# Performance work log

Hardware: AMD Instinct MI355X
Metric: run time of the kernel (lower is better)

The kernel has to match this reference:

```python
import jax, jax.numpy as jnp
import numpy as np

N = 12288
IN_DIM = 128
OUT_DIM = 128
LR_SLOPE = 0.01
NEG_INF = -9e16


def setup_inputs() -> dict:
    key = jax.random.key(0)
    k1, k2, k3, k4 = jax.random.split(key, 4)
    emb_mat = jax.random.normal(k1, (N, IN_DIM), dtype=jnp.float32)
    adj_mat = jax.random.randint(k2, (N, N), 0, 2, dtype=jnp.int32)
    # xavier-normal-ish init for params
    W = jax.random.normal(k3, (OUT_DIM, IN_DIM), dtype=jnp.float32) * (2.0 / (IN_DIM + OUT_DIM)) ** 0.5
    a = jax.random.normal(k4, (2 * OUT_DIM, 1), dtype=jnp.float32) * (2.0 / (2 * OUT_DIM + 1)) ** 0.5
    return {"emb_mat": emb_mat, "adj_mat": adj_mat, "W": W, "a": a}


def reference(emb_mat, adj_mat, W, a):
    out_dim = W.shape[0]
    e_new = emb_mat @ W.T                       # [N, D_out]
    a1 = a[:out_dim, :]                         # [D_out, 1]
    a2 = a[out_dim:, :]                         # [D_out, 1]
    source_scores = e_new @ a1                  # [N, 1]
    target_scores = e_new @ a2                  # [N, 1]
    e = source_scores + target_scores.T         # [N, N] outer sum
    e = jax.nn.leaky_relu(e, negative_slope=LR_SLOPE)
    e = jnp.where(adj_mat > 0, e, NEG_INF)
    attention = jax.nn.softmax(e, axis=-1)      # [N, N]
    e_transf = attention @ e_new                # [N, D_out]
    return jax.nn.relu(e_transf)
```

## Files before the change

### kernel.cpp

```cpp
#include <hip/hip_runtime.h>


#define NN 12288
#define DIM 128
#define CSPLIT 8
#define COLS_PER (NN / CSPLIT)
#define BK 32
#define NCHUNK (COLS_PER / BK)

typedef __bf16 bf16x8 __attribute__((ext_vector_type(8)));
typedef float f32x4 __attribute__((ext_vector_type(4)));

__global__ __launch_bounds__(256) void k1_gemm(const float* __restrict__ emb,
                                               const float* __restrict__ W,
                                               const float* __restrict__ a,
                                               __bf16* __restrict__ Vt,
                                               float* __restrict__ s,
                                               float* __restrict__ t) {
  const int lane = threadIdx.x & 63;
  const int wave = threadIdx.x >> 6;
  const int m = lane & 15;
  const int quad = lane >> 4;
  const int row0 = blockIdx.x * 64 + wave * 16;

  f32x4 acc[8];
#pragma unroll
  for (int nb = 0; nb < 8; nb++) acc[nb] = (f32x4){0.f, 0.f, 0.f, 0.f};

#pragma unroll
  for (int ks = 0; ks < 4; ks++) {
    const int k0 = ks * 32 + quad * 8;
    const float* ep = emb + (size_t)(row0 + m) * DIM + k0;
    float4 lo = *(const float4*)ep;
    float4 hi = *(const float4*)(ep + 4);
    bf16x8 af = {(__bf16)lo.x, (__bf16)lo.y, (__bf16)lo.z, (__bf16)lo.w,
                 (__bf16)hi.x, (__bf16)hi.y, (__bf16)hi.z, (__bf16)hi.w};
#pragma unroll
    for (int nb = 0; nb < 8; nb++) {
      const float* wp = W + (size_t)(nb * 16 + m) * DIM + k0;
      float4 wlo = *(const float4*)wp;
      float4 whi = *(const float4*)(wp + 4);
      bf16x8 bf = {(__bf16)wlo.x, (__bf16)wlo.y, (__bf16)wlo.z, (__bf16)wlo.w,
                   (__bf16)whi.x, (__bf16)whi.y, (__bf16)whi.z, (__bf16)whi.w};
      acc[nb] = __builtin_amdgcn_mfma_f32_16x16x32_bf16(af, bf, acc[nb], 0, 0, 0);
    }
  }

  float a1v[8], a2v[8];
#pragma unroll
  for (int nb = 0; nb < 8; nb++) {
    a1v[nb] = a[nb * 16 + m];
    a2v[nb] = a[DIM + nb * 16 + m];
  }
#pragma unroll
  for (int r = 0; r < 4; r++) {
    const int gr = row0 + quad * 4 + r;
    float ps = 0.f, pt = 0.f;
#pragma unroll
    for (int nb = 0; nb < 8; nb++) {
      float e = acc[nb][r];
      ps += e * a1v[nb];
      pt += e * a2v[nb];
      Vt[(size_t)(nb * 16 + m) * NN + gr] = (__bf16)e;
    }
    ps += __shfl_xor(ps, 1); ps += __shfl_xor(ps, 2);
    ps += __shfl_xor(ps, 4); ps += __shfl_xor(ps, 8);
    pt += __shfl_xor(pt, 1); pt += __shfl_xor(pt, 2);
    pt += __shfl_xor(pt, 4); pt += __shfl_xor(pt, 8);
    if (m == 0) { s[gr] = ps; t[gr] = pt; }
  }
}

__global__ __launch_bounds__(256) void ktmax(const float* __restrict__ t,
                                             float* __restrict__ tmax) {
  __shared__ float red[256];
  float mx = -1e30f;
  for (int i = threadIdx.x; i < NN; i += 256) mx = fmaxf(mx, t[i]);
  red[threadIdx.x] = mx;
  __syncthreads();
  for (int off = 128; off; off >>= 1) {
    if ((int)threadIdx.x < off) red[threadIdx.x] = fmaxf(red[threadIdx.x], red[threadIdx.x + off]);
    __syncthreads();
  }
  if (threadIdx.x == 0) *tmax = red[0];
}

__global__ __launch_bounds__(256, 3) void k2_attn(const int* __restrict__ adj,
                                                  const __bf16* __restrict__ Vt,
                                                  const float* __restrict__ s,
                                                  const float* __restrict__ t,
                                                  const float* __restrict__ tmaxp,
                                                  float* __restrict__ part,
                                                  float* __restrict__ lpart) {
  __shared__ unsigned long long adjb[2][128][5];
  __shared__ __attribute__((aligned(16))) __bf16 vtb[2][128][40];

  const int tid = threadIdx.x;
  const int lane = tid & 63;
  const int wave = tid >> 6;
  const int m = lane & 15;
  const int quad = lane >> 4;
  const int row0 = blockIdx.x * 128;
  const int cs = blockIdx.y;
  const int col0 = cs * COLS_PER;
  const int rowA = row0 + wave * 32 + m;
  const int rowB = rowA + 16;

  const float Tmax = *tmaxp;
  const float sA = s[rowA], sB = s[rowB];
  const float uA = sA + Tmax, uB = sB + Tmax;
  const float mA = fmaxf(uA, 0.01f * uA);
  const float mB = fmaxf(uB, 0.01f * uB);

  f32x4 accA[8], accB[8];
#pragma unroll
  for (int nb = 0; nb < 8; nb++) {
    accA[nb] = (f32x4){0.f, 0.f, 0.f, 0.f};
    accB[nb] = (f32x4){0.f, 0.f, 0.f, 0.f};
  }
  float lA = 0.f, lB = 0.f;

  int4 ga[4];
  bf16x8 gv[2];
  const int fr = tid >> 3, fc = (tid & 7) * 4;
  const int vd = tid >> 2, vc = (tid & 3) * 8;

  auto fetch = [&](int c) {
    const int cc = col0 + c * BK;
#pragma unroll
    for (int p = 0; p < 4; p++)
      ga[p] = *(const int4*)(adj + (size_t)(row0 + fr + p * 32) * NN + cc + fc);
#pragma unroll
    for (int p = 0; p < 2; p++)
      gv[p] = *(const bf16x8*)(Vt + (size_t)(vd + p * 64) * NN + cc + vc);
  };
  auto commit = [&](int b) {
#pragma unroll
    for (int p = 0; p < 4; p++) {
      unsigned pk = (unsigned)(ga[p].x != 0) | ((unsigned)(ga[p].y != 0) << 8) |
                    ((unsigned)(ga[p].z != 0) << 16) | ((unsigned)(ga[p].w != 0) << 24);
      *(unsigned*)((unsigned char*)&adjb[b][fr + p * 32][0] + fc) = pk;
    }
#pragma unroll
    for (int p = 0; p < 2; p++)
      *(bf16x8*)&vtb[b][vd + p * 64][vc] = gv[p];
  };

  fetch(0);
  commit(0);
  __syncthreads();

  for (int c = 0; c < NCHUNK; c++) {
    if (c + 1 < NCHUNK) fetch(c + 1);

    const int b = c & 1;
    const float* tp = t + col0 + c * BK + quad * 8;
    float4 ct0 = *(const float4*)tp;
    float4 ct1 = *(const float4*)(tp + 4);
    unsigned long long avA = adjb[b][wave * 32 + m][quad];
    unsigned long long avB = adjb[b][wave * 32 + 16 + m][quad];

    bf16x8 pA, pB;
#define PEL(frag, jj, tv, av, ss, mm, ll)                               \
    {                                                                   \
      float v = (ss) + (tv);                                            \
      float lv = fmaxf(v, 0.01f * v);                                   \
      float e = (((av) >> (8 * (jj))) & 1) ? __expf(lv - (mm)) : 0.f;   \
      (ll) += e;                                                        \
      frag[jj] = (__bf16)e;                                             \
    }
    PEL(pA, 0, ct0.x, avA, sA, mA, lA)
    PEL(pA, 1, ct0.y, avA, sA, mA, lA)
    PEL(pA, 2, ct0.z, avA, sA, mA, lA)
    PEL(pA, 3, ct0.w, avA, sA, mA, lA)
    PEL(pA, 4, ct1.x, avA, sA, mA, lA)
    PEL(pA, 5, ct1.y, avA, sA, mA, lA)
    PEL(pA, 6, ct1.z, avA, sA, mA, lA)
    PEL(pA, 7, ct1.w, avA, sA, mA, lA)
    PEL(pB, 0, ct0.x, avB, sB, mB, lB)
    PEL(pB, 1, ct0.y, avB, sB, mB, lB)
    PEL(pB, 2, ct0.z, avB, sB, mB, lB)
    PEL(pB, 3, ct0.w, avB, sB, mB, lB)
    PEL(pB, 4, ct1.x, avB, sB, mB, lB)
    PEL(pB, 5, ct1.y, avB, sB, mB, lB)
    PEL(pB, 6, ct1.z, avB, sB, mB, lB)
    PEL(pB, 7, ct1.w, avB, sB, mB, lB)
#undef PEL

#pragma unroll
    for (int nb = 0; nb < 8; nb++) {
      bf16x8 bv = *(const bf16x8*)&vtb[b][nb * 16 + m][quad * 8];
      accA[nb] = __builtin_amdgcn_mfma_f32_16x16x32_bf16(pA, bv, accA[nb], 0, 0, 0);
      accB[nb] = __builtin_amdgcn_mfma_f32_16x16x32_bf16(pB, bv, accB[nb], 0, 0, 0);
    }

    if (c + 1 < NCHUNK) commit((c + 1) & 1);
    __syncthreads();
  }

  lA += __shfl_xor(lA, 16); lA += __shfl_xor(lA, 32);
  lB += __shfl_xor(lB, 16); lB += __shfl_xor(lB, 32);
  if (quad == 0) {
    lpart[(size_t)cs * NN + rowA] = lA;
    lpart[(size_t)cs * NN + rowB] = lB;
  }

  float* po = part + ((size_t)cs * NN + row0 + wave * 32) * DIM;
#pragma unroll
  for (int nb = 0; nb < 8; nb++) {
#pragma unroll
    for (int r = 0; r < 4; r++) {
      po[(size_t)(quad * 4 + r) * DIM + nb * 16 + m] = accA[nb][r];
      po[(size_t)(16 + quad * 4 + r) * DIM + nb * 16 + m] = accB[nb][r];
    }
  }
}

__global__ __launch_bounds__(256) void kl(const float* __restrict__ lpart,
                                          float* __restrict__ linv) {
  const int r = blockIdx.x * 256 + threadIdx.x;
  float l = 0.f;
#pragma unroll
  for (int cs = 0; cs < CSPLIT; cs++) l += lpart[(size_t)cs * NN + r];
  linv[r] = 1.0f / l;
}

__global__ __launch_bounds__(256) void k3_fin(const float* __restrict__ part,
                                              const float* __restrict__ linv,
                                              float* __restrict__ out) {
  const int idx = blockIdx.x * 256 + threadIdx.x;
  const int row = idx >> 5;
  const float4* p4 = (const float4*)part;
  float4 acc = p4[idx];
#pragma unroll
  for (int cs = 1; cs < CSPLIT; cs++) {
    float4 v = p4[(size_t)cs * (NN * DIM / 4) + idx];
    acc.x += v.x; acc.y += v.y; acc.z += v.z; acc.w += v.w;
  }
  const float li = linv[row];
  float4 o;
  o.x = fmaxf(acc.x * li, 0.f);
  o.y = fmaxf(acc.y * li, 0.f);
  o.z = fmaxf(acc.z * li, 0.f);
  o.w = fmaxf(acc.w * li, 0.f);
  ((float4*)out)[idx] = o;
}

extern "C" void kernel_launch(void* const* d_in, const int* in_sizes, int n_in,
                              void* d_out, int out_size, void* d_ws, size_t ws_size,
                              hipStream_t stream) {
  (void)in_sizes; (void)n_in; (void)out_size; (void)ws_size;
  const float* emb = (const float*)d_in[0];
  const int* adj = (const int*)d_in[1];
  const float* W = (const float*)d_in[2];
  const float* a = (const float*)d_in[3];
  float* out = (float*)d_out;

  char* ws = (char*)d_ws;
  __bf16* Vt = (__bf16*)ws;
  float* s = (float*)(ws + 3145728);
  float* t = (float*)(ws + 3194880);
  float* lpart = (float*)(ws + 3244032);
  float* linv = (float*)(ws + 3637248);
  float* tmax = (float*)(ws + 3686400);
  float* part = (float*)(ws + 3686656);

  k1_gemm<<<NN / 64, 256, 0, stream>>>(emb, W, a, Vt, s, t);
  ktmax<<<1, 256, 0, stream>>>(t, tmax);
  dim3 g2(NN / 128, CSPLIT);
  k2_attn<<<g2, 256, 0, stream>>>(adj, Vt, s, t, tmax, part, lpart);
  kl<<<NN / 256, 256, 0, stream>>>(lpart, linv);
  k3_fin<<<NN * DIM / 4 / 256, 256, 0, stream>>>(part, linv, out);
}
```

Baseline: 823.3 us.

## Fuse tmax and l-reduction into neighbor kernels and deepen prefetch pipeline

Removes the single-block ktmax kernel by computing the column-score max with an atomicMax on a biased float-as-uint in k1, launched with one wave per block. The kl kernel is folded into k3_fin, which reduces the row sums in shared memory. k2_attn now prefetches two chunks ahead in registers, including the t values, and skips the final barrier. The aim is to cut launch and serial-kernel overhead and hide global latency, at the cost of more registers in k2 and a +64 bias that assumes t > -64 for the uint ordering.

```diff
diff --git a/kernel.cpp b/kernel.cpp
--- a/kernel.cpp
+++ b/kernel.cpp
@@ -11,17 +11,17 @@
 typedef __bf16 bf16x8 __attribute__((ext_vector_type(8)));
 typedef float f32x4 __attribute__((ext_vector_type(4)));
 
-__global__ __launch_bounds__(256) void k1_gemm(const float* __restrict__ emb,
-                                               const float* __restrict__ W,
-                                               const float* __restrict__ a,
-                                               __bf16* __restrict__ Vt,
-                                               float* __restrict__ s,
-                                               float* __restrict__ t) {
-  const int lane = threadIdx.x & 63;
-  const int wave = threadIdx.x >> 6;
+__global__ __launch_bounds__(64) void k1_gemm(const float* __restrict__ emb,
+                                              const float* __restrict__ W,
+                                              const float* __restrict__ a,
+                                              __bf16* __restrict__ Vt,
+                                              float* __restrict__ s,
+                                              float* __restrict__ t,
+                                              unsigned* __restrict__ tmax) {
+  const int lane = threadIdx.x;
   const int m = lane & 15;
   const int quad = lane >> 4;
-  const int row0 = blockIdx.x * 64 + wave * 16;
+  const int row0 = blockIdx.x * 16;
 
   f32x4 acc[8];
 #pragma unroll
@@ -52,6 +52,7 @@
     a1v[nb] = a[nb * 16 + m];
     a2v[nb] = a[DIM + nb * 16 + m];
   }
+  float tm_local = 0.f;
 #pragma unroll
   for (int r = 0; r < 4; r++) {
     const int gr = row0 + quad * 4 + r;
@@ -67,29 +68,20 @@
     ps += __shfl_xor(ps, 4); ps += __shfl_xor(ps, 8);
     pt += __shfl_xor(pt, 1); pt += __shfl_xor(pt, 2);
     pt += __shfl_xor(pt, 4); pt += __shfl_xor(pt, 8);
-    if (m == 0) { s[gr] = ps; t[gr] = pt; }
-  }
-}
-
-__global__ __launch_bounds__(256) void ktmax(const float* __restrict__ t,
-                                             float* __restrict__ tmax) {
-  __shared__ float red[256];
-  float mx = -1e30f;
-  for (int i = threadIdx.x; i < NN; i += 256) mx = fmaxf(mx, t[i]);
-  red[threadIdx.x] = mx;
-  __syncthreads();
-  for (int off = 128; off; off >>= 1) {
-    if ((int)threadIdx.x < off) red[threadIdx.x] = fmaxf(red[threadIdx.x], red[threadIdx.x + off]);
-    __syncthreads();
-  }
-  if (threadIdx.x == 0) *tmax = red[0];
+    if (m == 0) {
+      s[gr] = ps;
+      t[gr] = pt;
+      tm_local = fmaxf(tm_local, pt + 64.0f);
+    }
+  }
+  if (m == 0) atomicMax(tmax, __float_as_uint(tm_local));
 }
 
 __global__ __launch_bounds__(256, 3) void k2_attn(const int* __restrict__ adj,
                                                   const __bf16* __restrict__ Vt,
                                                   const float* __restrict__ s,
                                                   const float* __restrict__ t,
-                                                  const float* __restrict__ tmaxp,
+                                                  const unsigned* __restrict__ tmaxp,
                                                   float* __restrict__ part,
                                                   float* __restrict__ lpart) {
   __shared__ unsigned long long adjb[2][128][5];
@@ -106,7 +98,7 @@
   const int rowA = row0 + wave * 32 + m;
   const int rowB = rowA + 16;
 
-  const float Tmax = *tmaxp;
+  const float Tmax = __uint_as_float(*tmaxp) - 64.0f;
   const float sA = s[rowA], sB = s[rowB];
   const float uA = sA + Tmax, uB = sB + Tmax;
   const float mA = fmaxf(uA, 0.01f * uA);
@@ -120,45 +112,50 @@
   }
   float lA = 0.f, lB = 0.f;
 
-  int4 ga[4];
-  bf16x8 gv[2];
+  int4 ga[2][4];
+  bf16x8 gv[2][2];
+  float4 gt[2][2];
   const int fr = tid >> 3, fc = (tid & 7) * 4;
   const int vd = tid >> 2, vc = (tid & 3) * 8;
-
-  auto fetch = [&](int c) {
+  const float* tp0 = t + col0 + quad * 8;
+
+  auto fetch = [&](int c, int b) {
     const int cc = col0 + c * BK;
 #pragma unroll
     for (int p = 0; p < 4; p++)
-      ga[p] = *(const int4*)(adj + (size_t)(row0 + fr + p * 32) * NN + cc + fc);
+      ga[b][p] = *(const int4*)(adj + (size_t)(row0 + fr + p * 32) * NN + cc + fc);
 #pragma unroll
     for (int p = 0; p < 2; p++)
-      gv[p] = *(const bf16x8*)(Vt + (size_t)(vd + p * 64) * NN + cc + vc);
+      gv[b][p] = *(const bf16x8*)(Vt + (size_t)(vd + p * 64) * NN + cc + vc);
+    gt[b][0] = *(const float4*)(tp0 + c * BK);
+    gt[b][1] = *(const float4*)(tp0 + c * BK + 4);
   };
-  auto commit = [&](int b) {
+  auto commit = [&](int c, int b) {
+    const int lb = c & 1;
 #pragma unroll
     for (int p = 0; p < 4; p++) {
-      unsigned pk = (unsigned)(ga[p].x != 0) | ((unsigned)(ga[p].y != 0) << 8) |
-                    ((unsigned)(ga[p].z != 0) << 16) | ((unsigned)(ga[p].w != 0) << 24);
-      *(unsigned*)((unsigned char*)&adjb[b][fr + p * 32][0] + fc) = pk;
+      unsigned pk = (unsigned)(ga[b][p].x != 0) | ((unsigned)(ga[b][p].y != 0) << 8) |
+                    ((unsigned)(ga[b][p].z != 0) << 16) | ((unsigned)(ga[b][p].w != 0) << 24);
+      *(unsigned*)((unsigned char*)&adjb[lb][fr + p * 32][0] + fc) = pk;
     }
 #pragma unroll
     for (int p = 0; p < 2; p++)
-      *(bf16x8*)&vtb[b][vd + p * 64][vc] = gv[p];
+      *(bf16x8*)&vtb[lb][vd + p * 64][vc] = gv[b][p];
   };
 
-  fetch(0);
-  commit(0);
+  fetch(0, 0);
+  commit(0, 0);
+  fetch(1, 1);
   __syncthreads();
 
   for (int c = 0; c < NCHUNK; c++) {
-    if (c + 1 < NCHUNK) fetch(c + 1);
-
-    const int b = c & 1;
-    const float* tp = t + col0 + c * BK + quad * 8;
-    float4 ct0 = *(const float4*)tp;
-    float4 ct1 = *(const float4*)(tp + 4);
-    unsigned long long avA = adjb[b][wave * 32 + m][quad];
-    unsigned long long avB = adjb[b][wave * 32 + 16 + m][quad];
+    const int cur = c & 1;
+    float4 ct0 = gt[cur][0];
+    float4 ct1 = gt[cur][1];
+    if (c + 2 < NCHUNK) fetch(c + 2, cur);
+
+    unsigned long long avA = adjb[cur][wave * 32 + m][quad];
+    unsigned long long avB = adjb[cur][wave * 32 + 16 + m][quad];
 
     bf16x8 pA, pB;
 #define PEL(frag, jj, tv, av, ss, mm, ll)                               \
@@ -189,13 +186,15 @@
 
 #pragma unroll
     for (int nb = 0; nb < 8; nb++) {
-      bf16x8 bv = *(const bf16x8*)&vtb[b][nb * 16 + m][quad * 8];
+      bf16x8 bv = *(const bf16x8*)&vtb[cur][nb * 16 + m][quad * 8];
       accA[nb] = __builtin_amdgcn_mfma_f32_16x16x32_bf16(pA, bv, accA[nb], 0, 0, 0);
       accB[nb] = __builtin_amdgcn_mfma_f32_16x16x32_bf16(pB, bv, accB[nb], 0, 0, 0);
     }
 
-    if (c + 1 < NCHUNK) commit((c + 1) & 1);
-    __syncthreads();
+    if (c + 1 < NCHUNK) {
+      commit(c + 1, (c + 1) & 1);
+      __syncthreads();
+    }
   }
 
   lA += __shfl_xor(lA, 16); lA += __shfl_xor(lA, 32);
@@ -216,20 +215,19 @@
   }
 }
 
-__global__ __launch_bounds__(256) void kl(const float* __restrict__ lpart,
-                                          float* __restrict__ linv) {
-  const int r = blockIdx.x * 256 + threadIdx.x;
-  float l = 0.f;
-#pragma unroll
-  for (int cs = 0; cs < CSPLIT; cs++) l += lpart[(size_t)cs * NN + r];
-  linv[r] = 1.0f / l;
-}
-
 __global__ __launch_bounds__(256) void k3_fin(const float* __restrict__ part,
-                                              const float* __restrict__ linv,
+                                              const float* __restrict__ lpart,
                                               float* __restrict__ out) {
+  __shared__ float linv_s[8];
+  const int r0 = blockIdx.x * 8;
+  if (threadIdx.x < 8) {
+    float l = 0.f;
+#pragma unroll
+    for (int cs = 0; cs < CSPLIT; cs++) l += lpart[(size_t)cs * NN + r0 + threadIdx.x];
+    linv_s[threadIdx.x] = 1.0f / l;
+  }
+  __syncthreads();
   const int idx = blockIdx.x * 256 + threadIdx.x;
-  const int row = idx >> 5;
   const float4* p4 = (const float4*)part;
   float4 acc = p4[idx];
 #pragma unroll
@@ -237,7 +235,7 @@
     float4 v = p4[(size_t)cs * (NN * DIM / 4) + idx];
     acc.x += v.x; acc.y += v.y; acc.z += v.z; acc.w += v.w;
   }
-  const float li = linv[row];
+  const float li = linv_s[threadIdx.x >> 5];
   float4 o;
   o.x = fmaxf(acc.x * li, 0.f);
   o.y = fmaxf(acc.y * li, 0.f);
@@ -261,14 +259,12 @@
   float* s = (float*)(ws + 3145728);
   float* t = (float*)(ws + 3194880);
   float* lpart = (float*)(ws + 3244032);
-  float* linv = (float*)(ws + 3637248);
-  float* tmax = (float*)(ws + 3686400);
-  float* part = (float*)(ws + 3686656);
-
-  k1_gemm<<<NN / 64, 256, 0, stream>>>(emb, W, a, Vt, s, t);
-  ktmax<<<1, 256, 0, stream>>>(t, tmax);
+  unsigned* tmax = (unsigned*)(ws + 3637248);
+  float* part = (float*)(ws + 3637504);
+
+  hipMemsetAsync(tmax, 0, 4, stream);
+  k1_gemm<<<NN / 16, 64, 0, stream>>>(emb, W, a, Vt, s, t, tmax);
   dim3 g2(NN / 128, CSPLIT);
   k2_attn<<<g2, 256, 0, stream>>>(adj, Vt, s, t, tmax, part, lpart);
-  kl<<<NN / 256, 256, 0, stream>>>(lpart, linv);
-  k3_fin<<<NN * DIM / 4 / 256, 256, 0, stream>>>(part, linv, out);
-}
+  k3_fin<<<NN / 8, 256, 0, stream>>>(part, lpart, out);
+}
```

Result: slower. 1.678 ms (+103.9%).
